# Performance work log

Hardware: AMD Instinct MI355X
Metric: run time of the kernel (lower is better)

The kernel has to match this reference:

```python
import jax, jax.numpy as jnp
import numpy as np

B, L, D, E, TOP_K = 8, 1024, 768, 4, 2
H = 2 * D  # expert hidden dim
LN_EPS = 1e-5


def _gelu(v):
    return jax.nn.gelu(v, approximate=False)  # torch nn.GELU default (erf)


def _mish(v):
    return v * jnp.tanh(jax.nn.softplus(v))


_ACTS = [_gelu, jax.nn.silu, _mish, _gelu]  # per-expert activations from __init__


def setup_inputs() -> dict:
    key = jax.random.key(0)
    ks = jax.random.split(key, 8)
    x = jax.random.normal(ks[0], (B, L, D), dtype=jnp.float32)
    router_w = jax.random.normal(ks[1], (E, D), dtype=jnp.float32) * 0.02
    router_b = jnp.zeros((E,), dtype=jnp.float32)
    w1 = jax.random.normal(ks[2], (E, D, H), dtype=jnp.float32) * (1.0 / np.sqrt(D))
    b1 = jax.random.normal(ks[3], (E, H), dtype=jnp.float32) * 0.01
    w2 = jax.random.normal(ks[4], (E, H, D), dtype=jnp.float32) * (1.0 / np.sqrt(H))
    b2 = jax.random.normal(ks[5], (E, D), dtype=jnp.float32) * 0.01
    ln_g = jnp.ones((D,), dtype=jnp.float32)
    ln_b = jnp.zeros((D,), dtype=jnp.float32)
    return {"x": x, "router_w": router_w, "router_b": router_b,
            "w1": w1, "b1": b1, "w2": w2, "b2": b2,
            "ln_g": ln_g, "ln_b": ln_b}


def reference(x, router_w, router_b, w1, b1, w2, b2, ln_g, ln_b):
    # Eval-mode forward (no router noise, no dropout, no aux loss).
    b, l, d = x.shape
    e = router_w.shape[0]

    # Per-sample routing on mean-pooled features.
    pooled = x.mean(axis=1)                              # [B, D]
    logits = pooled @ router_w.T + router_b              # [B, E]
    top_v, top_i = jax.lax.top_k(logits, TOP_K)          # [B, K]
    gates_k = jax.nn.softmax(top_v, axis=-1)             # [B, K]
    # Dense gate matrix: mostly zero, 2 nonzeros per row (matches masked scatter).
    gate = jnp.zeros((b, e), x.dtype).at[jnp.arange(b)[:, None], top_i].add(gates_k)

    # All experts densely (per-sample gate zeros out unrouted experts).
    h = jnp.einsum('bld,edh->belh', x, w1) + b1[None, :, None, :]   # [B, E, L, 2D]
    h = jnp.stack([_ACTS[i](h[:, i]) for i in range(e)], axis=1)
    out = jnp.einsum('belh,ehd->beld', h, w2) + b2[None, :, None, :]  # [B, E, L, D]

    # Gated combine + residual, then LayerNorm.
    y = jnp.einsum('be,beld->bld', gate, out) + x
    mu = y.mean(axis=-1, keepdims=True)
    var = ((y - mu) ** 2).mean(axis=-1, keepdims=True)
    return (y - mu) * jax.lax.rsqrt(var + LN_EPS) * ln_g + ln_b
```

## Files before the change

kernel.cpp:

```cpp
#include <hip/hip_runtime.h>

#define B_ 8
#define L_ 1024
#define D_ 768
#define E_ 4
#define H_ 1536

typedef __attribute__((ext_vector_type(8))) short bf16x8;
typedef __attribute__((ext_vector_type(4))) float f32x4;

#define AS1 __attribute__((address_space(1)))
#define AS3 __attribute__((address_space(3)))

__device__ __forceinline__ unsigned short f2bf(float f) {
  unsigned int u = __float_as_uint(f);
  u += 0x7FFFu + ((u >> 16) & 1u);
  return (unsigned short)(u >> 16);
}
__device__ __forceinline__ float bf2f(unsigned short h) {
  return __uint_as_float(((unsigned int)h) << 16);
}

__device__ __forceinline__ float sigm(float z) {
  return __builtin_amdgcn_rcpf(1.0f + __builtin_amdgcn_exp2f(z * -1.442695040888963f));
}
__device__ __forceinline__ float act_fn(float v, int e) {
  if (e == 1) return v * sigm(v);
  if (e == 2) {
    float p = __builtin_amdgcn_exp2f(fminf(v, 30.0f) * 1.442695040888963f);
    float q = 1.0f + p, q2 = q * q;
    return v * (q2 - 1.0f) * __builtin_amdgcn_rcpf(q2 + 1.0f);
  }
  float u = v * (0.7978845608028654f + 0.0356774081f * v * v);
  return v * sigm(2.0f * u);
}

__global__ __launch_bounds__(192) void k_cvtx_pool(const float* __restrict__ x,
                                                   unsigned short* __restrict__ xbf,
                                                   float* __restrict__ part) {
  const int c = blockIdx.x;
  const int b = blockIdx.y;
  const int t = threadIdx.x;
  const float* xb = x + ((size_t)b * L_ + (size_t)c * 64) * D_;
  unsigned short* ob = xbf ? xbf + ((size_t)b * L_ + (size_t)c * 64) * D_ : nullptr;
  float4 s = make_float4(0.f, 0.f, 0.f, 0.f);
  for (int l = 0; l < 64; ++l) {
    float4 v = *(const float4*)(xb + (size_t)l * D_ + t * 4);
    s.x += v.x; s.y += v.y; s.z += v.z; s.w += v.w;
    if (ob)
      *(ushort4*)(ob + (size_t)l * D_ + t * 4) =
          make_ushort4(f2bf(v.x), f2bf(v.y), f2bf(v.z), f2bf(v.w));
  }
  *(float4*)(part + ((size_t)b * 16 + c) * D_ + t * 4) = s;
}

__global__ __launch_bounds__(256) void k_route(const float* __restrict__ part,
                                               const float* __restrict__ rw,
                                               const float* __restrict__ rb,
                                               int* __restrict__ slot_e,
                                               float* __restrict__ slot_g) {
  const int b = blockIdx.x;
  const int t = threadIdx.x;
  __shared__ float red[256][4];
  float p0 = 0.f, p1 = 0.f, p2 = 0.f;
  const float* pb = part + (size_t)b * 16 * D_;
  for (int c = 0; c < 16; ++c) {
    p0 += pb[c * D_ + t];
    p1 += pb[c * D_ + t + 256];
    p2 += pb[c * D_ + t + 512];
  }
  p0 *= (1.0f / L_); p1 *= (1.0f / L_); p2 *= (1.0f / L_);
  for (int e = 0; e < 4; ++e)
    red[t][e] = p0 * rw[e * D_ + t] + p1 * rw[e * D_ + t + 256] + p2 * rw[e * D_ + t + 512];
  __syncthreads();
  for (int s = 128; s > 0; s >>= 1) {
    if (t < s)
      for (int e = 0; e < 4; ++e) red[t][e] += red[t + s][e];
    __syncthreads();
  }
  if (t == 0) {
    float lg[4];
    for (int e = 0; e < 4; ++e) lg[e] = red[0][e] + rb[e];
    int i0 = 0;
    for (int e = 1; e < 4; ++e) if (lg[e] > lg[i0]) i0 = e;
    int i1 = -1;
    for (int e = 0; e < 4; ++e) {
      if (e == i0) continue;
      if (i1 < 0 || lg[e] > lg[i1]) i1 = e;
    }
    float ex = expf(lg[i1] - lg[i0]);
    slot_e[2 * b]     = i0; slot_g[2 * b]     = 1.0f / (1.0f + ex);
    slot_e[2 * b + 1] = i1; slot_g[2 * b + 1] = ex / (1.0f + ex);
  }
}

__global__ __launch_bounds__(256) void k_cvtw(const float* __restrict__ src,
                                              unsigned short* __restrict__ dst,
                                              int R, int C) {
  __shared__ float tile[32][33];
  const int e = blockIdx.z;
  const float* s = src + (size_t)e * R * C;
  unsigned short* d = dst + (size_t)e * R * C;
  const int c0 = blockIdx.x * 32, r0 = blockIdx.y * 32;
  const int tx = threadIdx.x & 31, ty = threadIdx.x >> 5;
#pragma unroll
  for (int i = 0; i < 32; i += 8)
    tile[ty + i][tx] = s[(size_t)(r0 + ty + i) * C + c0 + tx];
  __syncthreads();
  const int c = threadIdx.x >> 3, r4 = (threadIdx.x & 7) * 4;
  ushort4 o = make_ushort4(f2bf(tile[r4 + 0][c]), f2bf(tile[r4 + 1][c]),
                           f2bf(tile[r4 + 2][c]), f2bf(tile[r4 + 3][c]));
  *(ushort4*)&d[(size_t)(c0 + c) * R + r0 + r4] = o;
}

__device__ __forceinline__ void stage_tile(const unsigned short* __restrict__ src, int pitch,
                                           unsigned short* lds, int t) {
#pragma unroll
  for (int rnd = 0; rnd < 2; ++rnd) {
    const int o = rnd * 4096 + t * 16;
    const int row = o >> 6;
    const int kb = (o & 63) ^ (((row >> 1) & 3) << 4);
    const unsigned short* g = src + (size_t)row * pitch + (kb >> 1);
    unsigned short* d = lds + ((o & ~1023) >> 1);
    __builtin_amdgcn_global_load_lds((AS1 const void*)g, (AS3 void*)d, 16, 0, 0);
  }
}

__device__ __forceinline__ bf16x8 frag(const unsigned short* lds, int row, int kq8) {
  const int byte = (row << 6) + ((kq8 << 1) ^ (((row >> 1) & 3) << 4));
  return *(const bf16x8*)((const char*)lds + byte);
}

__device__ __forceinline__ void block_bar() {
  asm volatile("" ::: "memory");
  __builtin_amdgcn_s_barrier();
  asm volatile("" ::: "memory");
}

__global__ __launch_bounds__(256) void k_ffn1a(const unsigned short* __restrict__ xbf,
                                               const unsigned short* __restrict__ w1t,
                                               const float* __restrict__ b1,
                                               const int* __restrict__ slot_e,
                                               const float* __restrict__ slot_g,
                                               unsigned short* __restrict__ hact) {
  __shared__ char smem[49152];
  unsigned short (*Abuf)[4096] = (unsigned short(*)[4096])smem;
  unsigned short (*Bbuf)[4096] = (unsigned short(*)[4096])(smem + 24576);
  int wg = blockIdx.x;
  wg = (wg & 7) * 192 + (wg >> 3);
  const int hx = wg % 12;
  const int ly = (wg / 12) & 7;
  const int s  = wg / 96;
  const int e = slot_e[s];
  const float g = slot_g[s];
  const int b = s >> 1;
  const int l0 = ly * 128, h0 = hx * 128;
  const int t = threadIdx.x, lane = t & 63, w = t >> 6;
  const int wm = (w >> 1) * 64, wn = (w & 1) * 64;
  const int c16 = lane & 15, kq8 = (lane >> 4) * 8, rq = (lane >> 4) * 4;
  const unsigned short* A  = xbf + ((size_t)b * L_ + l0) * D_;
  const unsigned short* Bp = w1t + ((size_t)e * H_ + h0) * D_;
  f32x4 acc[4][4] = {};
  const int NT = D_ / 32;

  stage_tile(A,      D_, Abuf[0], t); stage_tile(Bp,      D_, Bbuf[0], t);
  stage_tile(A + 32, D_, Abuf[1], t); stage_tile(Bp + 32, D_, Bbuf[1], t);
  stage_tile(A + 64, D_, Abuf[2], t); stage_tile(Bp + 64, D_, Bbuf[2], t);
  int cb = 0;
  for (int kt = 0; kt < NT; ++kt) {
    if (kt + 3 <= NT)      asm volatile("s_waitcnt vmcnt(8)" ::: "memory");
    else if (kt + 2 == NT) asm volatile("s_waitcnt vmcnt(4)" ::: "memory");
    else                   asm volatile("s_waitcnt vmcnt(0)" ::: "memory");
    block_bar();
    const unsigned short* Ac = Abuf[cb];
    const unsigned short* Bc = Bbuf[cb];
    bf16x8 af[4], bfr[4];
#pragma unroll
    for (int i = 0; i < 4; ++i) af[i]  = frag(Ac, wm + i * 16 + c16, kq8);
#pragma unroll
    for (int i = 0; i < 4; ++i) bfr[i] = frag(Bc, wn + i * 16 + c16, kq8);
#pragma unroll
    for (int mi = 0; mi < 4; ++mi)
#pragma unroll
      for (int ni = 0; ni < 4; ++ni)
        acc[mi][ni] = __builtin_amdgcn_mfma_f32_16x16x32_bf16(af[mi], bfr[ni], acc[mi][ni], 0, 0, 0);
    block_bar();
    if (kt + 3 < NT) {
      stage_tile(A + (kt + 3) * 32,  D_, Abuf[cb], t);
      stage_tile(Bp + (kt + 3) * 32, D_, Bbuf[cb], t);
    }
    cb = (cb == 2) ? 0 : cb + 1;
  }

  const float* b1e = b1 + (size_t)e * H_;
  unsigned short* Cl = (unsigned short*)smem;
#pragma unroll
  for (int ni = 0; ni < 4; ++ni) {
    int n = wn + ni * 16 + c16;
    float bias = b1e[h0 + n];
#pragma unroll
    for (int mi = 0; mi < 4; ++mi)
#pragma unroll
      for (int j = 0; j < 4; ++j) {
        int m = wm + mi * 16 + rq + j;
        Cl[m * 136 + n] = f2bf(act_fn(acc[mi][ni][j] + bias, e) * g);
      }
  }
  __syncthreads();
  unsigned short* hs = hact + (((size_t)s * L_ + l0) * H_) + h0;
  const int rr = t >> 4, cc8 = (t & 15) * 8;
#pragma unroll
  for (int i = 0; i < 8; ++i) {
    int r = i * 16 + rr;
    *(bf16x8*)(hs + (size_t)r * H_ + cc8) = *(const bf16x8*)(Cl + r * 136 + cc8);
  }
}

__global__ __launch_bounds__(256) void k_ffn2a(const unsigned short* __restrict__ hact,
                                               const unsigned short* __restrict__ w2t,
                                               const float* __restrict__ b2,
                                               const int* __restrict__ slot_e,
                                               const float* __restrict__ slot_g,
                                               const float* __restrict__ x,
                                               float* __restrict__ y,
                                               unsigned short* __restrict__ ypart) {
  __shared__ char smem[49152];
  unsigned short (*Abuf)[4096] = (unsigned short(*)[4096])smem;
  unsigned short (*Bbuf)[4096] = (unsigned short(*)[4096])(smem + 24576);
  int wg = blockIdx.x;
  wg = (wg & 7) * 96 + (wg >> 3);
  const int dx = wg % 6;
  const int ly = (wg / 6) & 7;
  const int s  = wg / 48;
  const int si = s & 1, b = s >> 1;
  const int e = slot_e[s];
  const float g = slot_g[s];
  const int l0 = ly * 128, d0 = dx * 128;
  const int t = threadIdx.x, lane = t & 63, w = t >> 6;
  const int wm = (w >> 1) * 64, wn = (w & 1) * 64;
  const int c16 = lane & 15, kq8 = (lane >> 4) * 8, rq = (lane >> 4) * 4;
  const unsigned short* A  = hact + ((size_t)s * L_ + l0) * H_;
  const unsigned short* Bp = w2t + ((size_t)e * D_ + d0) * H_;
  f32x4 acc[4][4] = {};
  const int NT = H_ / 32;

  stage_tile(A,      H_, Abuf[0], t); stage_tile(Bp,      H_, Bbuf[0], t);
  stage_tile(A + 32, H_, Abuf[1], t); stage_tile(Bp + 32, H_, Bbuf[1], t);
  stage_tile(A + 64, H_, Abuf[2], t); stage_tile(Bp + 64, H_, Bbuf[2], t);
  int cb = 0;
  for (int kt = 0; kt < NT; ++kt) {
    if (kt + 3 <= NT)      asm volatile("s_waitcnt vmcnt(8)" ::: "memory");
    else if (kt + 2 == NT) asm volatile("s_waitcnt vmcnt(4)" ::: "memory");
    else                   asm volatile("s_waitcnt vmcnt(0)" ::: "memory");
    block_bar();
    const unsigned short* Ac = Abuf[cb];
    const unsigned short* Bc = Bbuf[cb];
    bf16x8 af[4], bfr[4];
#pragma unroll
    for (int i = 0; i < 4; ++i) af[i]  = frag(Ac, wm + i * 16 + c16, kq8);
#pragma unroll
    for (int i = 0; i < 4; ++i) bfr[i] = frag(Bc, wn + i * 16 + c16, kq8);
#pragma unroll
    for (int mi = 0; mi < 4; ++mi)
#pragma unroll
      for (int ni = 0; ni < 4; ++ni)
        acc[mi][ni] = __builtin_amdgcn_mfma_f32_16x16x32_bf16(af[mi], bfr[ni], acc[mi][ni], 0, 0, 0);
    block_bar();
    if (kt + 3 < NT) {
      stage_tile(A + (kt + 3) * 32,  H_, Abuf[cb], t);
      stage_tile(Bp + (kt + 3) * 32, H_, Bbuf[cb], t);
    }
    cb = (cb == 2) ? 0 : cb + 1;
  }

  if (si == 0) {
    const float* xb = x + (size_t)b * L_ * D_;
    float* yb = y + (size_t)b * L_ * D_;
#pragma unroll
    for (int ni = 0; ni < 4; ++ni) {
      int n = d0 + wn + ni * 16 + c16;
      float bias = g * b2[(size_t)e * D_ + n];
#pragma unroll
      for (int mi = 0; mi < 4; ++mi)
#pragma unroll
        for (int j = 0; j < 4; ++j) {
          int m = l0 + wm + mi * 16 + rq + j;
          yb[(size_t)m * D_ + n] = acc[mi][ni][j] + bias + xb[(size_t)m * D_ + n];
        }
    }
  } else {
    unsigned short* Cl = (unsigned short*)smem;
#pragma unroll
    for (int ni = 0; ni < 4; ++ni) {
      int n = wn + ni * 16 + c16;
      float bias = g * b2[(size_t)e * D_ + d0 + n];
#pragma unroll
      for (int mi = 0; mi < 4; ++mi)
#pragma unroll
        for (int j = 0; j < 4; ++j) {
          int m = wm + mi * 16 + rq + j;
          Cl[m * 136 + n] = f2bf(acc[mi][ni][j] + bias);
        }
    }
    __syncthreads();
    unsigned short* yp = ypart + ((size_t)b * L_ + l0) * D_ + d0;
    const int rr = t >> 4, cc8 = (t & 15) * 8;
#pragma unroll
    for (int i = 0; i < 8; ++i) {
      int r = i * 16 + rr;
      *(bf16x8*)(yp + (size_t)r * D_ + cc8) = *(const bf16x8*)(Cl + r * 136 + cc8);
    }
  }
}

__global__ __launch_bounds__(256) void k_ln(float* __restrict__ y,
                                            const unsigned short* __restrict__ yp,
                                            const float* __restrict__ g,
                                            const float* __restrict__ bt) {
  const int t = threadIdx.x;
  const int row = blockIdx.x * 4 + (t >> 6);
  const int lane = t & 63;
  float* yr = y + (size_t)row * D_;
  float4 v[3];
  float sum = 0.f;
#pragma unroll
  for (int i = 0; i < 3; ++i) {
    v[i] = *(const float4*)(yr + i * 256 + lane * 4);
    if (yp) {
      ushort4 p = *(const ushort4*)(yp + (size_t)row * D_ + i * 256 + lane * 4);
      v[i].x += bf2f(p.x); v[i].y += bf2f(p.y); v[i].z += bf2f(p.z); v[i].w += bf2f(p.w);
    }
    sum += v[i].x + v[i].y + v[i].z + v[i].w;
  }
#pragma unroll
  for (int off = 32; off > 0; off >>= 1) sum += __shfl_xor(sum, off);
  const float mu = sum * (1.0f / D_);
  float var = 0.f;
#pragma unroll
  for (int i = 0; i < 3; ++i) {
    v[i].x -= mu; v[i].y -= mu; v[i].z -= mu; v[i].w -= mu;
    var += v[i].x * v[i].x + v[i].y * v[i].y + v[i].z * v[i].z + v[i].w * v[i].w;
  }
#pragma unroll
  for (int off = 32; off > 0; off >>= 1) var += __shfl_xor(var, off);
  const float rstd = rsqrtf(var * (1.0f / D_) + 1e-5f);
#pragma unroll
  for (int i = 0; i < 3; ++i) {
    float4 gg = *(const float4*)(g + i * 256 + lane * 4);
    float4 bb = *(const float4*)(bt + i * 256 + lane * 4);
    float4 o;
    o.x = v[i].x * rstd * gg.x + bb.x;
    o.y = v[i].y * rstd * gg.y + bb.y;
    o.z = v[i].z * rstd * gg.z + bb.z;
    o.w = v[i].w * rstd * gg.w + bb.w;
    *(float4*)(yr + i * 256 + lane * 4) = o;
  }
}

__global__ __launch_bounds__(256) void k_ffn1b(const float* __restrict__ x,
                                               const float* __restrict__ w1,
                                               const float* __restrict__ b1,
                                               const int* __restrict__ slot_e,
                                               const float* __restrict__ slot_g,
                                               unsigned short* __restrict__ hact) {
  __shared__ unsigned short Al[128][40];
  __shared__ unsigned short Bl[128][40];
  const int s = blockIdx.z;
  const int e = slot_e[s];
  const float g = slot_g[s];
  const int b = s >> 1;
  const int l0 = blockIdx.y * 128, h0 = blockIdx.x * 128;
  const int t = threadIdx.x, lane = t & 63, w = t >> 6;
  const int wm = (w >> 1) * 64, wn = (w & 1) * 64;
  const int c16 = lane & 15, kq = (lane >> 4) * 8, rq = (lane >> 4) * 4;
  const int ar = t >> 3, ac = (t & 7) * 4;
  const int bn = t & 127, bk0 = (t >> 7) * 4;
  const float* xb  = x  + (size_t)b * L_ * D_;
  const float* w1e = w1 + (size_t)e * D_ * H_;
  f32x4 acc[4][4] = {};
  for (int k0 = 0; k0 < D_; k0 += 32) {
#pragma unroll
    for (int p = 0; p < 4; ++p) {
      int r = p * 32 + ar;
      float4 v = *(const float4*)(xb + (size_t)(l0 + r) * D_ + (k0 + ac));
      *(ushort4*)&Al[r][ac] = make_ushort4(f2bf(v.x), f2bf(v.y), f2bf(v.z), f2bf(v.w));
    }
#pragma unroll
    for (int p = 0; p < 4; ++p) {
      int kk = bk0 + p * 8;
      const float* src = w1e + (size_t)(k0 + kk) * H_ + (h0 + bn);
      *(ushort4*)&Bl[bn][kk] = make_ushort4(f2bf(src[0]), f2bf(src[H_]), f2bf(src[2 * H_]), f2bf(src[3 * H_]));
    }
    __syncthreads();
    bf16x8 af[4], bfr[4];
#pragma unroll
    for (int i = 0; i < 4; ++i) af[i]  = *(const bf16x8*)&Al[wm + i * 16 + c16][kq];
#pragma unroll
    for (int i = 0; i < 4; ++i) bfr[i] = *(const bf16x8*)&Bl[wn + i * 16 + c16][kq];
#pragma unroll
    for (int mi = 0; mi < 4; ++mi)
#pragma unroll
      for (int ni = 0; ni < 4; ++ni)
        acc[mi][ni] = __builtin_amdgcn_mfma_f32_16x16x32_bf16(af[mi], bfr[ni], acc[mi][ni], 0, 0, 0);
    __syncthreads();
  }
  const float* b1e = b1 + (size_t)e * H_;
  unsigned short* hs = hact + (size_t)s * L_ * H_;
#pragma unroll
  for (int ni = 0; ni < 4; ++ni) {
    int n = h0 + wn + ni * 16 + c16;
    float bias = b1e[n];
#pragma unroll
    for (int mi = 0; mi < 4; ++mi)
#pragma unroll
      for (int j = 0; j < 4; ++j) {
        int m = l0 + wm + mi * 16 + rq + j;
        hs[(size_t)m * H_ + n] = f2bf(act_fn(acc[mi][ni][j] + bias, e) * g);
      }
  }
}

__global__ __launch_bounds__(256) void k_ffn2b(const unsigned short* __restrict__ hact,
                                               const float* __restrict__ w2,
                                               const float* __restrict__ b2,
                                               const int* __restrict__ slot_e,
                                               const float* __restrict__ slot_g,
                                               const float* __restrict__ x,
                                               float* __restrict__ y) {
  __shared__ unsigned short Al[128][40];
  __shared__ unsigned short Bl[128][40];
  const int b = blockIdx.z;
  const int l0 = blockIdx.y * 128, d0 = blockIdx.x * 128;
  const int t = threadIdx.x, lane = t & 63, w = t >> 6;
  const int wm = (w >> 1) * 64, wn = (w & 1) * 64;
  const int c16 = lane & 15, kq = (lane >> 4) * 8, rq = (lane >> 4) * 4;
  const int ar = t >> 3, ac = (t & 7) * 4;
  const int bn = t & 127, bk0 = (t >> 7) * 4;
  f32x4 acc[4][4] = {};
  for (int si = 0; si < 2; ++si) {
    const int s = 2 * b + si;
    const int e = slot_e[s];
    const unsigned short* hs = hact + (size_t)s * L_ * H_;
    const float* w2e = w2 + (size_t)e * H_ * D_;
    for (int k0 = 0; k0 < H_; k0 += 32) {
#pragma unroll
      for (int p = 0; p < 4; ++p) {
        int r = p * 32 + ar;
        *(ushort4*)&Al[r][ac] = *(const ushort4*)(hs + (size_t)(l0 + r) * H_ + (k0 + ac));
      }
#pragma unroll
      for (int p = 0; p < 4; ++p) {
        int kk = bk0 + p * 8;
        const float* src = w2e + (size_t)(k0 + kk) * D_ + (d0 + bn);
        *(ushort4*)&Bl[bn][kk] = make_ushort4(f2bf(src[0]), f2bf(src[D_]), f2bf(src[2 * D_]), f2bf(src[3 * D_]));
      }
      __syncthreads();
      bf16x8 af[4], bfr[4];
#pragma unroll
      for (int i = 0; i < 4; ++i) af[i]  = *(const bf16x8*)&Al[wm + i * 16 + c16][kq];
#pragma unroll
      for (int i = 0; i < 4; ++i) bfr[i] = *(const bf16x8*)&Bl[wn + i * 16 + c16][kq];
#pragma unroll
      for (int mi = 0; mi < 4; ++mi)
#pragma unroll
        for (int ni = 0; ni < 4; ++ni)
          acc[mi][ni] = __builtin_amdgcn_mfma_f32_16x16x32_bf16(af[mi], bfr[ni], acc[mi][ni], 0, 0, 0);
      __syncthreads();
    }
  }
  const int e0 = slot_e[2 * b], e1 = slot_e[2 * b + 1];
  const float g0 = slot_g[2 * b], g1 = slot_g[2 * b + 1];
  const float* xb = x + (size_t)b * L_ * D_;
  float* yb = y + (size_t)b * L_ * D_;
#pragma unroll
  for (int ni = 0; ni < 4; ++ni) {
    int n = d0 + wn + ni * 16 + c16;
    float bias = g0 * b2[e0 * D_ + n] + g1 * b2[e1 * D_ + n];
#pragma unroll
    for (int mi = 0; mi < 4; ++mi)
#pragma unroll
      for (int j = 0; j < 4; ++j) {
        int m = l0 + wm + mi * 16 + rq + j;
        yb[(size_t)m * D_ + n] = acc[mi][ni][j] + bias + xb[(size_t)m * D_ + n];
      }
  }
}

__global__ __launch_bounds__(256) void k_ln_b(float* __restrict__ y,
                                              const float* __restrict__ g,
                                              const float* __restrict__ bt) {
  const int t = threadIdx.x;
  const int row = blockIdx.x * 4 + (t >> 6);
  const int lane = t & 63;
  float* yr = y + (size_t)row * D_;
  float4 v[3];
  float sum = 0.f;
#pragma unroll
  for (int i = 0; i < 3; ++i) {
    v[i] = *(const float4*)(yr + i * 256 + lane * 4);
    sum += v[i].x + v[i].y + v[i].z + v[i].w;
  }
#pragma unroll
  for (int off = 32; off > 0; off >>= 1) sum += __shfl_xor(sum, off);
  const float mu = sum * (1.0f / D_);
  float var = 0.f;
#pragma unroll
  for (int i = 0; i < 3; ++i) {
    v[i].x -= mu; v[i].y -= mu; v[i].z -= mu; v[i].w -= mu;
    var += v[i].x * v[i].x + v[i].y * v[i].y + v[i].z * v[i].z + v[i].w * v[i].w;
  }
#pragma unroll
  for (int off = 32; off > 0; off >>= 1) var += __shfl_xor(var, off);
  const float rstd = rsqrtf(var * (1.0f / D_) + 1e-5f);
#pragma unroll
  for (int i = 0; i < 3; ++i) {
    float4 gg = *(const float4*)(g + i * 256 + lane * 4);
    float4 bb = *(const float4*)(bt + i * 256 + lane * 4);
    float4 o;
    o.x = v[i].x * rstd * gg.x + bb.x;
    o.y = v[i].y * rstd * gg.y + bb.y;
    o.z = v[i].z * rstd * gg.z + bb.z;
    o.w = v[i].w * rstd * gg.w + bb.w;
    *(float4*)(yr + i * 256 + lane * 4) = o;
  }
}

extern "C" void kernel_launch(void* const* d_in, const int* in_sizes, int n_in,
                              void* d_out, int out_size, void* d_ws, size_t ws_size,
                              hipStream_t stream) {
  const float* x  = (const float*)d_in[0];
  const float* rw = (const float*)d_in[1];
  const float* rb = (const float*)d_in[2];
  const float* w1 = (const float*)d_in[3];
  const float* b1 = (const float*)d_in[4];
  const float* w2 = (const float*)d_in[5];
  const float* b2 = (const float*)d_in[6];
  const float* lg = (const float*)d_in[7];
  const float* lb = (const float*)d_in[8];
  float* y = (float*)d_out;

  char* ws = (char*)d_ws;
  int*   slot_e = (int*)ws;
  float* slot_g = (float*)(ws + 64);
  float* part   = (float*)(ws + 256);

  const size_t OFF_XBF  = 524288ull;
  const size_t OFF_WBUF = OFF_XBF + 12582912ull;
  const size_t OFF_HACT = OFF_WBUF + 9437184ull;
  const size_t NEED_A   = OFF_HACT + 50331648ull;

  if (ws_size >= NEED_A) {
    unsigned short* xbf   = (unsigned short*)(ws + OFF_XBF);
    unsigned short* wbuf  = (unsigned short*)(ws + OFF_WBUF);
    unsigned short* hact  = (unsigned short*)(ws + OFF_HACT);
    unsigned short* ypart = (unsigned short*)(ws + OFF_XBF);

    k_cvtx_pool<<<dim3(16, 8), 192, 0, stream>>>(x, xbf, part);
    k_route    <<<8,           256, 0, stream>>>(part, rw, rb, slot_e, slot_g);
    k_cvtw     <<<dim3(48, 24, 4), 256, 0, stream>>>(w1, wbuf, D_, H_);
    k_ffn1a    <<<1536, 256, 0, stream>>>(xbf, wbuf, b1, slot_e, slot_g, hact);
    k_cvtw     <<<dim3(24, 48, 4), 256, 0, stream>>>(w2, wbuf, H_, D_);
    k_ffn2a    <<<768,  256, 0, stream>>>(hact, wbuf, b2, slot_e, slot_g, x, y, ypart);
    k_ln       <<<2048, 256, 0, stream>>>(y, ypart, lg, lb);
  } else {
    unsigned short* hact = (unsigned short*)(ws + (1 << 19));
    k_cvtx_pool<<<dim3(16, 8), 192, 0, stream>>>(x, nullptr, part);
    k_route    <<<8,           256, 0, stream>>>(part, rw, rb, slot_e, slot_g);
    k_ffn1b    <<<dim3(12, 8, 16), 256, 0, stream>>>(x, w1, b1, slot_e, slot_g, hact);
    k_ffn2b    <<<dim3(6, 8, 8),   256, 0, stream>>>(hact, w2, b2, slot_e, slot_g, x, y);
    k_ln_b     <<<2048,        256, 0, stream>>>(y, lg, lb);
  }
}
```

Before: 171.5 us.

## Merge x conversion, pooling and both weight casts into one prologue kernel; inline routing

Replaces the separate pool, route and two weight-conversion kernels with a single k_pre launch that converts x to bf16, computes partial sums, and transposes/casts both w1 and w2 into separate buffers. Each FFN workgroup now recomputes the routing decision redundantly from the partial sums instead of reading from a route kernel. This cuts the launch count and the serialization between small kernels, at the cost of redundant per-block routing work (a reduction plus barriers before the GEMM prologue) and an extra workspace region for w2t. The fallback path is adjusted to use k_ln with a null ypart.

```diff
diff --git a/kernel.cpp b/kernel.cpp
--- a/kernel.cpp
+++ b/kernel.cpp
@@ -35,73 +35,13 @@
   return v * sigm(2.0f * u);
 }
 
-__global__ __launch_bounds__(192) void k_cvtx_pool(const float* __restrict__ x,
-                                                   unsigned short* __restrict__ xbf,
-                                                   float* __restrict__ part) {
-  const int c = blockIdx.x;
-  const int b = blockIdx.y;
-  const int t = threadIdx.x;
-  const float* xb = x + ((size_t)b * L_ + (size_t)c * 64) * D_;
-  unsigned short* ob = xbf ? xbf + ((size_t)b * L_ + (size_t)c * 64) * D_ : nullptr;
-  float4 s = make_float4(0.f, 0.f, 0.f, 0.f);
-  for (int l = 0; l < 64; ++l) {
-    float4 v = *(const float4*)(xb + (size_t)l * D_ + t * 4);
-    s.x += v.x; s.y += v.y; s.z += v.z; s.w += v.w;
-    if (ob)
-      *(ushort4*)(ob + (size_t)l * D_ + t * 4) =
-          make_ushort4(f2bf(v.x), f2bf(v.y), f2bf(v.z), f2bf(v.w));
-  }
-  *(float4*)(part + ((size_t)b * 16 + c) * D_ + t * 4) = s;
-}
-
-__global__ __launch_bounds__(256) void k_route(const float* __restrict__ part,
-                                               const float* __restrict__ rw,
-                                               const float* __restrict__ rb,
-                                               int* __restrict__ slot_e,
-                                               float* __restrict__ slot_g) {
-  const int b = blockIdx.x;
-  const int t = threadIdx.x;
-  __shared__ float red[256][4];
-  float p0 = 0.f, p1 = 0.f, p2 = 0.f;
-  const float* pb = part + (size_t)b * 16 * D_;
-  for (int c = 0; c < 16; ++c) {
-    p0 += pb[c * D_ + t];
-    p1 += pb[c * D_ + t + 256];
-    p2 += pb[c * D_ + t + 512];
-  }
-  p0 *= (1.0f / L_); p1 *= (1.0f / L_); p2 *= (1.0f / L_);
-  for (int e = 0; e < 4; ++e)
-    red[t][e] = p0 * rw[e * D_ + t] + p1 * rw[e * D_ + t + 256] + p2 * rw[e * D_ + t + 512];
-  __syncthreads();
-  for (int s = 128; s > 0; s >>= 1) {
-    if (t < s)
-      for (int e = 0; e < 4; ++e) red[t][e] += red[t + s][e];
-    __syncthreads();
-  }
-  if (t == 0) {
-    float lg[4];
-    for (int e = 0; e < 4; ++e) lg[e] = red[0][e] + rb[e];
-    int i0 = 0;
-    for (int e = 1; e < 4; ++e) if (lg[e] > lg[i0]) i0 = e;
-    int i1 = -1;
-    for (int e = 0; e < 4; ++e) {
-      if (e == i0) continue;
-      if (i1 < 0 || lg[e] > lg[i1]) i1 = e;
-    }
-    float ex = expf(lg[i1] - lg[i0]);
-    slot_e[2 * b]     = i0; slot_g[2 * b]     = 1.0f / (1.0f + ex);
-    slot_e[2 * b + 1] = i1; slot_g[2 * b + 1] = ex / (1.0f + ex);
-  }
-}
-
-__global__ __launch_bounds__(256) void k_cvtw(const float* __restrict__ src,
-                                              unsigned short* __restrict__ dst,
-                                              int R, int C) {
-  __shared__ float tile[32][33];
-  const int e = blockIdx.z;
+__device__ __forceinline__ void cvtw_body(const float* __restrict__ src,
+                                          unsigned short* __restrict__ dst,
+                                          int R, int C, int bx, int by, int e,
+                                          float (*tile)[33]) {
   const float* s = src + (size_t)e * R * C;
   unsigned short* d = dst + (size_t)e * R * C;
-  const int c0 = blockIdx.x * 32, r0 = blockIdx.y * 32;
+  const int c0 = bx * 32, r0 = by * 32;
   const int tx = threadIdx.x & 31, ty = threadIdx.x >> 5;
 #pragma unroll
   for (int i = 0; i < 32; i += 8)
@@ -113,6 +53,99 @@
   *(ushort4*)&d[(size_t)(c0 + c) * R + r0 + r4] = o;
 }
 
+__global__ __launch_bounds__(256) void k_pre(const float* __restrict__ x,
+                                             unsigned short* __restrict__ xbf,
+                                             float* __restrict__ part,
+                                             const float* __restrict__ w1,
+                                             unsigned short* __restrict__ w1t,
+                                             const float* __restrict__ w2,
+                                             unsigned short* __restrict__ w2t) {
+  __shared__ float tile[32][33];
+  int bid = blockIdx.x;
+  if (bid < 128) {
+    const int t = threadIdx.x;
+    if (t >= 192) return;
+    const int c = bid & 15, b = bid >> 4;
+    const float* xb = x + ((size_t)b * L_ + (size_t)c * 64) * D_;
+    unsigned short* ob = xbf + ((size_t)b * L_ + (size_t)c * 64) * D_;
+    float4 s = make_float4(0.f, 0.f, 0.f, 0.f);
+    for (int l = 0; l < 64; ++l) {
+      float4 v = *(const float4*)(xb + (size_t)l * D_ + t * 4);
+      s.x += v.x; s.y += v.y; s.z += v.z; s.w += v.w;
+      *(ushort4*)(ob + (size_t)l * D_ + t * 4) =
+          make_ushort4(f2bf(v.x), f2bf(v.y), f2bf(v.z), f2bf(v.w));
+    }
+    *(float4*)(part + ((size_t)b * 16 + c) * D_ + t * 4) = s;
+    return;
+  }
+  bid -= 128;
+  if (bid < 4608) {
+    cvtw_body(w1, w1t, D_, H_, bid % 48, (bid / 48) % 24, bid / 1152, tile);
+    return;
+  }
+  bid -= 4608;
+  cvtw_body(w2, w2t, H_, D_, bid % 24, (bid / 24) % 48, bid / 1152, tile);
+}
+
+__global__ __launch_bounds__(256) void k_cvtw(const float* __restrict__ src,
+                                              unsigned short* __restrict__ dst,
+                                              int R, int C) {
+  __shared__ float tile[32][33];
+  cvtw_body(src, dst, R, C, blockIdx.x, blockIdx.y, blockIdx.z, tile);
+}
+
+__device__ __forceinline__ void route_block(const float* __restrict__ part,
+                                            const float* __restrict__ rw,
+                                            const float* __restrict__ rb,
+                                            int s, float* red, int t,
+                                            int& e_out, float& g_out) {
+  const int b = s >> 1, si = s & 1;
+  float p0 = 0.f, p1 = 0.f, p2 = 0.f;
+  const float* pb = part + (size_t)b * 16 * D_;
+  for (int c = 0; c < 16; ++c) {
+    p0 += pb[c * D_ + t];
+    p1 += pb[c * D_ + t + 256];
+    p2 += pb[c * D_ + t + 512];
+  }
+  p0 *= (1.0f / L_); p1 *= (1.0f / L_); p2 *= (1.0f / L_);
+  for (int e = 0; e < 4; ++e)
+    red[t * 4 + e] = p0 * rw[e * D_ + t] + p1 * rw[e * D_ + t + 256] + p2 * rw[e * D_ + t + 512];
+  __syncthreads();
+  for (int ss = 128; ss > 0; ss >>= 1) {
+    if (t < ss)
+      for (int e = 0; e < 4; ++e) red[t * 4 + e] += red[(t + ss) * 4 + e];
+    __syncthreads();
+  }
+  float lg[4];
+  for (int e = 0; e < 4; ++e) lg[e] = red[e] + rb[e];
+  int i0 = 0;
+  for (int e = 1; e < 4; ++e) if (lg[e] > lg[i0]) i0 = e;
+  int i1 = -1;
+  for (int e = 0; e < 4; ++e) {
+    if (e == i0) continue;
+    if (i1 < 0 || lg[e] > lg[i1]) i1 = e;
+  }
+  float ex = expf(lg[i1] - lg[i0]);
+  if (si == 0) { e_out = i0; g_out = 1.0f / (1.0f + ex); }
+  else         { e_out = i1; g_out = ex / (1.0f + ex); }
+  __syncthreads();
+}
+
+__global__ __launch_bounds__(256) void k_route(const float* __restrict__ part,
+                                               const float* __restrict__ rw,
+                                               const float* __restrict__ rb,
+                                               int* __restrict__ slot_e,
+                                               float* __restrict__ slot_g) {
+  __shared__ float red[256 * 4];
+  int e0, e1; float g0, g1;
+  route_block(part, rw, rb, 2 * (int)blockIdx.x,     red, threadIdx.x, e0, g0);
+  route_block(part, rw, rb, 2 * (int)blockIdx.x + 1, red, threadIdx.x, e1, g1);
+  if (threadIdx.x == 0) {
+    slot_e[2 * blockIdx.x] = e0;     slot_g[2 * blockIdx.x] = g0;
+    slot_e[2 * blockIdx.x + 1] = e1; slot_g[2 * blockIdx.x + 1] = g1;
+  }
+}
+
 __device__ __forceinline__ void stage_tile(const unsigned short* __restrict__ src, int pitch,
                                            unsigned short* lds, int t) {
 #pragma unroll
@@ -140,8 +173,9 @@
 __global__ __launch_bounds__(256) void k_ffn1a(const unsigned short* __restrict__ xbf,
                                                const unsigned short* __restrict__ w1t,
                                                const float* __restrict__ b1,
-                                               const int* __restrict__ slot_e,
-                                               const float* __restrict__ slot_g,
+                                               const float* __restrict__ part,
+                                               const float* __restrict__ rw,
+                                               const float* __restrict__ rb,
                                                unsigned short* __restrict__ hact) {
   __shared__ char smem[49152];
   unsigned short (*Abuf)[4096] = (unsigned short(*)[4096])smem;
@@ -151,11 +185,11 @@
   const int hx = wg % 12;
   const int ly = (wg / 12) & 7;
   const int s  = wg / 96;
-  const int e = slot_e[s];
-  const float g = slot_g[s];
+  const int t = threadIdx.x, lane = t & 63, w = t >> 6;
+  int e; float g;
+  route_block(part, rw, rb, s, (float*)smem, t, e, g);
   const int b = s >> 1;
   const int l0 = ly * 128, h0 = hx * 128;
-  const int t = threadIdx.x, lane = t & 63, w = t >> 6;
   const int wm = (w >> 1) * 64, wn = (w & 1) * 64;
   const int c16 = lane & 15, kq8 = (lane >> 4) * 8, rq = (lane >> 4) * 4;
   const unsigned short* A  = xbf + ((size_t)b * L_ + l0) * D_;
@@ -219,8 +253,9 @@
 __global__ __launch_bounds__(256) void k_ffn2a(const unsigned short* __restrict__ hact,
                                                const unsigned short* __restrict__ w2t,
                                                const float* __restrict__ b2,
-                                               const int* __restrict__ slot_e,
-                                               const float* __restrict__ slot_g,
+                                               const float* __restrict__ part,
+                                               const float* __restrict__ rw,
+                                               const float* __restrict__ rb,
                                                const float* __restrict__ x,
                                                float* __restrict__ y,
                                                unsigned short* __restrict__ ypart) {
@@ -232,11 +267,11 @@
   const int dx = wg % 6;
   const int ly = (wg / 6) & 7;
   const int s  = wg / 48;
+  const int t = threadIdx.x, lane = t & 63, w = t >> 6;
+  int e; float g;
+  route_block(part, rw, rb, s, (float*)smem, t, e, g);
   const int si = s & 1, b = s >> 1;
-  const int e = slot_e[s];
-  const float g = slot_g[s];
   const int l0 = ly * 128, d0 = dx * 128;
-  const int t = threadIdx.x, lane = t & 63, w = t >> 6;
   const int wm = (w >> 1) * 64, wn = (w & 1) * 64;
   const int c16 = lane & 15, kq8 = (lane >> 4) * 8, rq = (lane >> 4) * 4;
   const unsigned short* A  = hact + ((size_t)s * L_ + l0) * H_;
@@ -355,6 +390,18 @@
     o.w = v[i].w * rstd * gg.w + bb.w;
     *(float4*)(yr + i * 256 + lane * 4) = o;
   }
+}
+
+__global__ __launch_bounds__(192) void k_poolb(const float* __restrict__ x,
+                                               float* __restrict__ part) {
+  const int c = blockIdx.x, b = blockIdx.y, t = threadIdx.x;
+  const float* xb = x + ((size_t)b * L_ + (size_t)c * 64) * D_;
+  float4 s = make_float4(0.f, 0.f, 0.f, 0.f);
+  for (int l = 0; l < 64; ++l) {
+    float4 v = *(const float4*)(xb + (size_t)l * D_ + t * 4);
+    s.x += v.x; s.y += v.y; s.z += v.z; s.w += v.w;
+  }
+  *(float4*)(part + ((size_t)b * 16 + c) * D_ + t * 4) = s;
 }
 
 __global__ __launch_bounds__(256) void k_ffn1b(const float* __restrict__ x,
@@ -486,45 +533,6 @@
   }
 }
 
-__global__ __launch_bounds__(256) void k_ln_b(float* __restrict__ y,
-                                              const float* __restrict__ g,
-                                              const float* __restrict__ bt) {
-  const int t = threadIdx.x;
-  const int row = blockIdx.x * 4 + (t >> 6);
-  const int lane = t & 63;
-  float* yr = y + (size_t)row * D_;
-  float4 v[3];
-  float sum = 0.f;
-#pragma unroll
-  for (int i = 0; i < 3; ++i) {
-    v[i] = *(const float4*)(yr + i * 256 + lane * 4);
-    sum += v[i].x + v[i].y + v[i].z + v[i].w;
-  }
-#pragma unroll
-  for (int off = 32; off > 0; off >>= 1) sum += __shfl_xor(sum, off);
-  const float mu = sum * (1.0f / D_);
-  float var = 0.f;
-#pragma unroll
-  for (int i = 0; i < 3; ++i) {
-    v[i].x -= mu; v[i].y -= mu; v[i].z -= mu; v[i].w -= mu;
-    var += v[i].x * v[i].x + v[i].y * v[i].y + v[i].z * v[i].z + v[i].w * v[i].w;
-  }
-#pragma unroll
-  for (int off = 32; off > 0; off >>= 1) var += __shfl_xor(var, off);
-  const float rstd = rsqrtf(var * (1.0f / D_) + 1e-5f);
-#pragma unroll
-  for (int i = 0; i < 3; ++i) {
-    float4 gg = *(const float4*)(g + i * 256 + lane * 4);
-    float4 bb = *(const float4*)(bt + i * 256 + lane * 4);
-    float4 o;
-    o.x = v[i].x * rstd * gg.x + bb.x;
-    o.y = v[i].y * rstd * gg.y + bb.y;
-    o.z = v[i].z * rstd * gg.z + bb.z;
-    o.w = v[i].w * rstd * gg.w + bb.w;
-    *(float4*)(yr + i * 256 + lane * 4) = o;
-  }
-}
-
 extern "C" void kernel_launch(void* const* d_in, const int* in_sizes, int n_in,
                               void* d_out, int out_size, void* d_ws, size_t ws_size,
                               hipStream_t stream) {
@@ -548,6 +556,8 @@
   const size_t OFF_WBUF = OFF_XBF + 12582912ull;
   const size_t OFF_HACT = OFF_WBUF + 9437184ull;
   const size_t NEED_A   = OFF_HACT + 50331648ull;
+  const size_t OFF_W2T  = NEED_A;
+  const size_t NEED_A2  = NEED_A + 9437184ull;
 
   if (ws_size >= NEED_A) {
     unsigned short* xbf   = (unsigned short*)(ws + OFF_XBF);
@@ -555,19 +565,25 @@
     unsigned short* hact  = (unsigned short*)(ws + OFF_HACT);
     unsigned short* ypart = (unsigned short*)(ws + OFF_XBF);
 
-    k_cvtx_pool<<<dim3(16, 8), 192, 0, stream>>>(x, xbf, part);
-    k_route    <<<8,           256, 0, stream>>>(part, rw, rb, slot_e, slot_g);
-    k_cvtw     <<<dim3(48, 24, 4), 256, 0, stream>>>(w1, wbuf, D_, H_);
-    k_ffn1a    <<<1536, 256, 0, stream>>>(xbf, wbuf, b1, slot_e, slot_g, hact);
-    k_cvtw     <<<dim3(24, 48, 4), 256, 0, stream>>>(w2, wbuf, H_, D_);
-    k_ffn2a    <<<768,  256, 0, stream>>>(hact, wbuf, b2, slot_e, slot_g, x, y, ypart);
-    k_ln       <<<2048, 256, 0, stream>>>(y, ypart, lg, lb);
+    if (ws_size >= NEED_A2) {
+      unsigned short* w2t = (unsigned short*)(ws + OFF_W2T);
+      k_pre  <<<128 + 4608 + 4608, 256, 0, stream>>>(x, xbf, part, w1, wbuf, w2, w2t);
+      k_ffn1a<<<1536, 256, 0, stream>>>(xbf, wbuf, b1, part, rw, rb, hact);
+      k_ffn2a<<<768,  256, 0, stream>>>(hact, w2t, b2, part, rw, rb, x, y, ypart);
+      k_ln   <<<2048, 256, 0, stream>>>(y, ypart, lg, lb);
+    } else {
+      k_pre  <<<128 + 4608, 256, 0, stream>>>(x, xbf, part, w1, wbuf, w2, nullptr);
+      k_ffn1a<<<1536, 256, 0, stream>>>(xbf, wbuf, b1, part, rw, rb, hact);
+      k_cvtw <<<dim3(24, 48, 4), 256, 0, stream>>>(w2, wbuf, H_, D_);
+      k_ffn2a<<<768,  256, 0, stream>>>(hact, wbuf, b2, part, rw, rb, x, y, ypart);
+      k_ln   <<<2048, 256, 0, stream>>>(y, ypart, lg, lb);
+    }
   } else {
     unsigned short* hact = (unsigned short*)(ws + (1 << 19));
-    k_cvtx_pool<<<dim3(16, 8), 192, 0, stream>>>(x, nullptr, part);
-    k_route    <<<8,           256, 0, stream>>>(part, rw, rb, slot_e, slot_g);
-    k_ffn1b    <<<dim3(12, 8, 16), 256, 0, stream>>>(x, w1, b1, slot_e, slot_g, hact);
-    k_ffn2b    <<<dim3(6, 8, 8),   256, 0, stream>>>(hact, w2, b2, slot_e, slot_g, x, y);
-    k_ln_b     <<<2048,        256, 0, stream>>>(y, lg, lb);
-  }
-}
+    k_poolb<<<dim3(16, 8), 192, 0, stream>>>(x, part);
+    k_route<<<8,           256, 0, stream>>>(part, rw, rb, slot_e, slot_g);
+    k_ffn1b<<<dim3(12, 8, 16), 256, 0, stream>>>(x, w1, b1, slot_e, slot_g, hact);
+    k_ffn2b<<<dim3(6, 8, 8),   256, 0, stream>>>(hact, w2, b2, slot_e, slot_g, x, y);
+    k_ln   <<<2048,        256, 0, stream>>>(y, nullptr, lg, lb);
+  }
+}
```

Result: faster. 151.2 us (-11.8%).
